# Performance work log

Hardware: AMD Instinct MI355X
Metric: run time of the kernel (lower is better)

## Reference

```python
import jax, jax.numpy as jnp
import numpy as np

EPS_BN = 1e-5
EPS_NORM = 1e-12


def _l2norm_c(x):
    # F.normalize over channel dim (dim=1) of [n, d, h, w]
    n = jnp.sqrt(jnp.sum(x * x, axis=1, keepdims=True))
    return x / jnp.maximum(n, EPS_NORM)


def setup_inputs() -> dict:
    key = jax.random.key(0)
    ks = jax.random.split(key, 8)
    g, p, d, h, w = 64, 64, 512, 24, 8
    hw = h * w
    return {
        "gal_fea": jax.random.normal(ks[0], (g, d, h, w), dtype=jnp.float32),
        "prob_fea": jax.random.normal(ks[1], (p, d, h, w), dtype=jnp.float32),
        "bn_weight": jax.random.uniform(ks[2], (1,), dtype=jnp.float32) + 0.5,
        "bn_bias": jax.random.uniform(ks[3], (1,), dtype=jnp.float32) - 0.5,
        "bn_mean": jnp.zeros((1,), dtype=jnp.float32),
        "bn_var": jnp.ones((1,), dtype=jnp.float32),
        "fc_weight": jax.random.normal(ks[4], (1, 2 * hw), dtype=jnp.float32) * 0.05,
        "fc_bias": jax.random.normal(ks[5], (1,), dtype=jnp.float32) * 0.05,
        "lbn_weight": jax.random.uniform(ks[6], (1,), dtype=jnp.float32) + 0.5,
        "lbn_bias": jax.random.uniform(ks[7], (1,), dtype=jnp.float32) - 0.5,
        "lbn_mean": jnp.zeros((1,), dtype=jnp.float32),
        "lbn_var": jnp.ones((1,), dtype=jnp.float32),
    }


def reference(gal_fea, prob_fea, bn_weight, bn_bias, bn_mean, bn_var,
              fc_weight, fc_bias, lbn_weight, lbn_bias, lbn_mean, lbn_var):
    g, d, h, w = gal_fea.shape
    p = prob_fea.shape[0]
    hw = h * w

    # L2-normalize over channels, flatten spatial dims
    gal = _l2norm_c(gal_fea).reshape(g, d, hw)              # [g, d, j]
    ker = _l2norm_c(prob_fea).transpose(0, 2, 3, 1).reshape(p, hw, d)  # [p, i, d]

    # cosine-similarity cross-correlation: s[g,p,i,j] = <probe pos i, gallery pos j>
    s = jnp.einsum('pid,gdj->gpij', ker, gal)               # [g, p, hw, hw]

    # dual spatial max-pool: max over probe positions, max over gallery positions
    score = jnp.concatenate([s.max(axis=2), s.max(axis=3)], axis=-1)  # [g, p, 2*hw]

    # eval-mode BatchNorm1d(1): scalar affine broadcast over all elements
    score = (score - bn_mean) / jnp.sqrt(bn_var + EPS_BN) * bn_weight + bn_bias

    # fc: Linear(2*hw, 1)
    score = jnp.einsum('gpk,ok->gpo', score, fc_weight)[..., 0] + fc_bias[0]  # [g, p]

    # eval-mode logit BatchNorm1d(1): scalar affine
    score = (score - lbn_mean) / jnp.sqrt(lbn_var + EPS_BN) * lbn_weight + lbn_bias

    return jax.nn.sigmoid(score / 10.0)
```

## Files before the change

kernel.cpp:

```cpp
#include <hip/hip_runtime.h>

#define HW 192
#define DD 512
#define GG 64
#define PP 64
#define SLAB 98304

typedef __attribute__((ext_vector_type(4))) float floatx4;
typedef __attribute__((ext_vector_type(2))) long long2_t;

typedef __attribute__((address_space(3))) unsigned int lds_u32;
typedef const __attribute__((address_space(1))) unsigned int glb_u32;

__device__ __forceinline__ void gload_lds16(const void* g, void* l) {
  __builtin_amdgcn_global_load_lds((glb_u32*)g, (lds_u32*)l, 16, 0, 0);
}

__global__ __launch_bounds__(512, 2) void norm_kernel(
    const float* __restrict__ gal, const float* __restrict__ prob,
    unsigned char* __restrict__ ws) {
  int b = blockIdx.x;
  int s = b / 12;
  int q = b - s * 12;
  const float* in = (s < GG) ? (gal + (size_t)s * DD * HW)
                             : (prob + (size_t)(s - GG) * DD * HW);
  unsigned char* out = ws + (size_t)s * SLAB;
  int pos0 = q * 16;
  int t = threadIdx.x;

  __shared__ float T[16][524];
  __shared__ float sqa[128][17];
  __shared__ float sq2[16][17];
  __shared__ float scl[16];

  {
    int cq = t >> 2;
    int quad = t & 3;
    float p0 = 0.f, p1 = 0.f, p2 = 0.f, p3 = 0.f;
#pragma unroll
    for (int cb = 0; cb < 4; ++cb) {
      int c = cb * 128 + cq;
      const float4 v = *(const float4*)(in + (size_t)c * HW + pos0 + quad * 4);
      T[quad * 4 + 0][c] = v.x;
      T[quad * 4 + 1][c] = v.y;
      T[quad * 4 + 2][c] = v.z;
      T[quad * 4 + 3][c] = v.w;
      p0 += v.x * v.x; p1 += v.y * v.y; p2 += v.z * v.z; p3 += v.w * v.w;
    }
    sqa[cq][quad * 4 + 0] = p0;
    sqa[cq][quad * 4 + 1] = p1;
    sqa[cq][quad * 4 + 2] = p2;
    sqa[cq][quad * 4 + 3] = p3;
  }
  __syncthreads();
  if (t < 256) {
    int g2 = t >> 4, pos = t & 15;
    float v = 0.f;
#pragma unroll
    for (int r = 0; r < 8; ++r) v += sqa[g2 * 8 + r][pos];
    sq2[g2][pos] = v;
  }
  __syncthreads();
  if (t < 16) {
    float v = 0.f;
#pragma unroll
    for (int r = 0; r < 16; ++r) v += sq2[r][t];
    scl[t] = 1.f / fmaxf(sqrtf(v), 1e-12f);
  }
  __syncthreads();

  {
    int kc = t & 3;
    int pos = (t >> 2) & 15;
    int kb2 = t >> 6;
    float sc = scl[pos];
    int base = kb2 * 64 + kc * 8;
    const float4 r0 = *(const float4*)&T[pos][base + 0];
    const float4 r1 = *(const float4*)&T[pos][base + 4];
    const float4 r2 = *(const float4*)&T[pos][base + 32];
    const float4 r3 = *(const float4*)&T[pos][base + 36];
    uint4 u;
    u.x = __builtin_amdgcn_cvt_pk_fp8_f32(r0.x * sc, r0.y * sc, 0, false);
    u.x = __builtin_amdgcn_cvt_pk_fp8_f32(r0.z * sc, r0.w * sc, u.x, true);
    u.y = __builtin_amdgcn_cvt_pk_fp8_f32(r1.x * sc, r1.y * sc, 0, false);
    u.y = __builtin_amdgcn_cvt_pk_fp8_f32(r1.z * sc, r1.w * sc, u.y, true);
    u.z = __builtin_amdgcn_cvt_pk_fp8_f32(r2.x * sc, r2.y * sc, 0, false);
    u.z = __builtin_amdgcn_cvt_pk_fp8_f32(r2.z * sc, r2.w * sc, u.z, true);
    u.w = __builtin_amdgcn_cvt_pk_fp8_f32(r3.x * sc, r3.y * sc, 0, false);
    u.w = __builtin_amdgcn_cvt_pk_fp8_f32(r3.z * sc, r3.w * sc, u.w, true);
    *(uint4*)(out + (size_t)kb2 * 12288 + (size_t)(pos0 + pos) * 64 + kc * 16) = u;
  }
}

__global__ __launch_bounds__(256, 2) void qaconv_gemm(
    const unsigned char* __restrict__ ws, const float* __restrict__ fcw,
    const float* __restrict__ bnw, const float* __restrict__ bnb,
    const float* __restrict__ bnm, const float* __restrict__ bnv,
    const float* __restrict__ fcb, const float* __restrict__ lw,
    const float* __restrict__ lb, const float* __restrict__ lm,
    const float* __restrict__ lv, float* __restrict__ out) {
  int bid = blockIdx.x;
  int sb = bid >> 6, li = bid & 63;
  int g = ((sb >> 3) << 3) + (li >> 3);
  int p = ((sb & 7) << 3) + (li & 7);
  const unsigned char* Bsrc = ws + (size_t)g * SLAB;
  const unsigned char* Asrc = ws + (size_t)(GG + p) * SLAB;

  __shared__ unsigned char A_lds[2][12288];
  __shared__ unsigned char B_lds[2][12288];
  __shared__ float colpart[2][HW];
  __shared__ float rowpart[2][HW];
  __shared__ float redbuf[4][2];

  int tid = threadIdx.x;
  int lane = tid & 63;
  int wave = tid >> 6;
  int wi = wave >> 1, wj = wave & 1;
  int l15 = lane & 15, l4 = lane >> 4;

  floatx4 acc[6][6];
#pragma unroll
  for (int a = 0; a < 6; ++a)
#pragma unroll
    for (int c = 0; c < 6; ++c) acc[a][c] = (floatx4){0.f, 0.f, 0.f, 0.f};

  int mIdx[3];
  int mOff[3];
#pragma unroll
  for (int s = 0; s < 3; ++s) {
    int m = tid + s * 256;
    mIdx[s] = m;
    mOff[s] = (m >> 2) * 64 + ((((m & 3) ^ ((m >> 3) & 3))) << 4);
  }

#define STAGE(KB2, BUF)                                             \
  do {                                                              \
    _Pragma("unroll") for (int s_ = 0; s_ < 3; ++s_) {              \
      size_t go = (size_t)(KB2)*12288 + (size_t)mOff[s_];           \
      gload_lds16(Asrc + go, &A_lds[BUF][mIdx[s_] * 16]);           \
      gload_lds16(Bsrc + go, &B_lds[BUF][mIdx[s_] * 16]);           \
    }                                                               \
  } while (0)

  STAGE(0, 0);
  __syncthreads();

  int sw = (l4 ^ ((l15 >> 1) & 3)) << 4;
  int aB = (wi * 96 + l15) * 64 + sw;
  int bB = (wj * 96 + l15) * 64 + sw;

  for (int kb2 = 0; kb2 < 8; ++kb2) {
    int cur = kb2 & 1;
    if (kb2 < 7) STAGE(kb2 + 1, cur ^ 1);

    long2_t a2[6];
#pragma unroll
    for (int it = 0; it < 6; ++it)
      a2[it] = *(const long2_t*)&A_lds[cur][aB + it * 1024];
#pragma unroll
    for (int jt = 0; jt < 6; ++jt) {
      long2_t b2 = *(const long2_t*)&B_lds[cur][bB + jt * 1024];
#pragma unroll
      for (int it = 0; it < 6; ++it)
        acc[it][jt] = __builtin_amdgcn_mfma_f32_16x16x32_fp8_fp8(a2[it].x, b2.x, acc[it][jt], 0, 0, 0);
#pragma unroll
      for (int it = 0; it < 6; ++it)
        acc[it][jt] = __builtin_amdgcn_mfma_f32_16x16x32_fp8_fp8(a2[it].y, b2.y, acc[it][jt], 0, 0, 0);
    }
    __syncthreads();
  }
#undef STAGE

  float cm[6];
  float rm[6][4];
#pragma unroll
  for (int jt = 0; jt < 6; ++jt) cm[jt] = -3.4e38f;
#pragma unroll
  for (int it = 0; it < 6; ++it)
#pragma unroll
    for (int r = 0; r < 4; ++r) rm[it][r] = -3.4e38f;
#pragma unroll
  for (int it = 0; it < 6; ++it)
#pragma unroll
    for (int jt = 0; jt < 6; ++jt)
#pragma unroll
      for (int r = 0; r < 4; ++r) {
        float v = acc[it][jt][r];
        cm[jt] = fmaxf(cm[jt], v);
        rm[it][r] = fmaxf(rm[it][r], v);
      }

#pragma unroll
  for (int jt = 0; jt < 6; ++jt) {
    float v = cm[jt];
    v = fmaxf(v, __shfl_xor(v, 16, 64));
    v = fmaxf(v, __shfl_xor(v, 32, 64));
    if (lane < 16) colpart[wi][wj * 96 + jt * 16 + lane] = v;
  }
#pragma unroll
  for (int it = 0; it < 6; ++it)
#pragma unroll
    for (int r = 0; r < 4; ++r) {
      float v = rm[it][r];
      v = fmaxf(v, __shfl_xor(v, 1, 64));
      v = fmaxf(v, __shfl_xor(v, 2, 64));
      v = fmaxf(v, __shfl_xor(v, 4, 64));
      v = fmaxf(v, __shfl_xor(v, 8, 64));
      if (l15 == 0) rowpart[wj][wi * 96 + it * 16 + l4 * 4 + r] = v;
    }
  __syncthreads();

  float part = 0.f, wpart = 0.f;
  if (tid < HW) {
    float cmax = fmaxf(colpart[0][tid], colpart[1][tid]);
    float rmax = fmaxf(rowpart[0][tid], rowpart[1][tid]);
    float w1 = fcw[tid], w2 = fcw[HW + tid];
    part = cmax * w1 + rmax * w2;
    wpart = w1 + w2;
  }
#pragma unroll
  for (int off = 32; off > 0; off >>= 1) {
    part += __shfl_down(part, off, 64);
    wpart += __shfl_down(wpart, off, 64);
  }
  if (lane == 0) { redbuf[wave][0] = part; redbuf[wave][1] = wpart; }
  __syncthreads();
  if (tid == 0) {
    float s = redbuf[0][0] + redbuf[1][0] + redbuf[2][0] + redbuf[3][0];
    float wsum = redbuf[0][1] + redbuf[1][1] + redbuf[2][1] + redbuf[3][1];
    float bnA = bnw[0] * rsqrtf(bnv[0] + 1e-5f);
    float bnB = bnb[0] - bnm[0] * bnA;
    float sc = bnA * s + bnB * wsum + fcb[0];
    float lA = lw[0] * rsqrtf(lv[0] + 1e-5f);
    sc = (sc - lm[0]) * lA + lb[0];
    out[g * PP + p] = 1.f / (1.f + __expf(-sc * 0.1f));
  }
}

extern "C" void kernel_launch(void* const* d_in, const int* in_sizes, int n_in,
                              void* d_out, int out_size, void* d_ws, size_t ws_size,
                              hipStream_t stream) {
  const float* gal  = (const float*)d_in[0];
  const float* prob = (const float*)d_in[1];
  const float* bnw  = (const float*)d_in[2];
  const float* bnb  = (const float*)d_in[3];
  const float* bnm  = (const float*)d_in[4];
  const float* bnv  = (const float*)d_in[5];
  const float* fcw  = (const float*)d_in[6];
  const float* fcb  = (const float*)d_in[7];
  const float* lw   = (const float*)d_in[8];
  const float* lb   = (const float*)d_in[9];
  const float* lm   = (const float*)d_in[10];
  const float* lv   = (const float*)d_in[11];
  unsigned char* ws = (unsigned char*)d_ws;
  float* out = (float*)d_out;

  hipLaunchKernelGGL(norm_kernel, dim3(1536), dim3(512), 0, stream, gal, prob, ws);
  hipLaunchKernelGGL(qaconv_gemm, dim3(GG * PP), dim3(256), 0, stream, ws, fcw,
                     bnw, bnb, bnm, bnv, fcb, lw, lb, lm, lv, out);
}
```

Before: 229.9 us.

## Switch fp8 GEMM to 32x32x64 scaled MFMA with matching fp8 layout

Replaces the 16x16x32 fp8 MFMA tiling (6x6 tiles per wave) with the gfx950 32x32x64 scaled f8f6f4 MFMA (3x3 tiles per wave), using unit scales. The norm kernel's fp8 packing order and the LDS read offsets change so each lane loads 32 contiguous k-bytes. The row/column max epilogue is rewritten for the 32x32 accumulator layout. The aim is fewer MFMA issues and LDS reads per k-step, at the cost of a more intricate layout mapping that must stay consistent between the two kernels.

```diff
diff --git a/kernel.cpp b/kernel.cpp
--- a/kernel.cpp
+++ b/kernel.cpp
@@ -6,8 +6,9 @@
 #define PP 64
 #define SLAB 98304
 
-typedef __attribute__((ext_vector_type(4))) float floatx4;
-typedef __attribute__((ext_vector_type(2))) long long2_t;
+typedef __attribute__((ext_vector_type(4))) int intx4;
+typedef __attribute__((ext_vector_type(8))) int intx8;
+typedef __attribute__((ext_vector_type(16))) float floatx16;
 
 typedef __attribute__((address_space(3))) unsigned int lds_u32;
 typedef const __attribute__((address_space(1))) unsigned int glb_u32;
@@ -74,11 +75,11 @@
     int pos = (t >> 2) & 15;
     int kb2 = t >> 6;
     float sc = scl[pos];
-    int base = kb2 * 64 + kc * 8;
+    int base = kb2 * 64 + kc * 16;
     const float4 r0 = *(const float4*)&T[pos][base + 0];
     const float4 r1 = *(const float4*)&T[pos][base + 4];
-    const float4 r2 = *(const float4*)&T[pos][base + 32];
-    const float4 r3 = *(const float4*)&T[pos][base + 36];
+    const float4 r2 = *(const float4*)&T[pos][base + 8];
+    const float4 r3 = *(const float4*)&T[pos][base + 12];
     uint4 u;
     u.x = __builtin_amdgcn_cvt_pk_fp8_f32(r0.x * sc, r0.y * sc, 0, false);
     u.x = __builtin_amdgcn_cvt_pk_fp8_f32(r0.z * sc, r0.w * sc, u.x, true);
@@ -116,13 +117,13 @@
   int lane = tid & 63;
   int wave = tid >> 6;
   int wi = wave >> 1, wj = wave & 1;
-  int l15 = lane & 15, l4 = lane >> 4;
-
-  floatx4 acc[6][6];
-#pragma unroll
-  for (int a = 0; a < 6; ++a)
-#pragma unroll
-    for (int c = 0; c < 6; ++c) acc[a][c] = (floatx4){0.f, 0.f, 0.f, 0.f};
+  int l31 = lane & 31;
+
+  floatx16 acc[3][3];
+#pragma unroll
+  for (int a = 0; a < 3; ++a)
+#pragma unroll
+    for (int c = 0; c < 3; ++c) acc[a][c] = (floatx16)(0.f);
 
   int mIdx[3];
   int mOff[3];
@@ -145,68 +146,69 @@
   STAGE(0, 0);
   __syncthreads();
 
-  int sw = (l4 ^ ((l15 >> 1) & 3)) << 4;
-  int aB = (wi * 96 + l15) * 64 + sw;
-  int bB = (wj * 96 + l15) * 64 + sw;
+  int xk = (lane >> 1) & 3;
+  int h2 = (lane >> 5) << 1;
+  int slotB0 = (h2 ^ xk) << 4;
+  int aO[3], bO[3];
+#pragma unroll
+  for (int ta = 0; ta < 3; ++ta) aO[ta] = (wi * 96 + ta * 32 + l31) * 64 + slotB0;
+#pragma unroll
+  for (int tc = 0; tc < 3; ++tc) bO[tc] = (wj * 96 + tc * 32 + l31) * 64 + slotB0;
+
+  const int sc8 = 0x7f7f7f7f;
 
   for (int kb2 = 0; kb2 < 8; ++kb2) {
     int cur = kb2 & 1;
     if (kb2 < 7) STAGE(kb2 + 1, cur ^ 1);
 
-    long2_t a2[6];
-#pragma unroll
-    for (int it = 0; it < 6; ++it)
-      a2[it] = *(const long2_t*)&A_lds[cur][aB + it * 1024];
-#pragma unroll
-    for (int jt = 0; jt < 6; ++jt) {
-      long2_t b2 = *(const long2_t*)&B_lds[cur][bB + jt * 1024];
-#pragma unroll
-      for (int it = 0; it < 6; ++it)
-        acc[it][jt] = __builtin_amdgcn_mfma_f32_16x16x32_fp8_fp8(a2[it].x, b2.x, acc[it][jt], 0, 0, 0);
-#pragma unroll
-      for (int it = 0; it < 6; ++it)
-        acc[it][jt] = __builtin_amdgcn_mfma_f32_16x16x32_fp8_fp8(a2[it].y, b2.y, acc[it][jt], 0, 0, 0);
+    intx8 af[3];
+#pragma unroll
+    for (int ta = 0; ta < 3; ++ta) {
+      intx4 lo = *(const intx4*)&A_lds[cur][aO[ta]];
+      intx4 hi = *(const intx4*)&A_lds[cur][aO[ta] ^ 16];
+      intx8 v;
+      v[0] = lo.x; v[1] = lo.y; v[2] = lo.z; v[3] = lo.w;
+      v[4] = hi.x; v[5] = hi.y; v[6] = hi.z; v[7] = hi.w;
+      af[ta] = v;
+    }
+#pragma unroll
+    for (int tc = 0; tc < 3; ++tc) {
+      intx4 lo = *(const intx4*)&B_lds[cur][bO[tc]];
+      intx4 hi = *(const intx4*)&B_lds[cur][bO[tc] ^ 16];
+      intx8 bf;
+      bf[0] = lo.x; bf[1] = lo.y; bf[2] = lo.z; bf[3] = lo.w;
+      bf[4] = hi.x; bf[5] = hi.y; bf[6] = hi.z; bf[7] = hi.w;
+#pragma unroll
+      for (int ta = 0; ta < 3; ++ta)
+        acc[ta][tc] = __builtin_amdgcn_mfma_scale_f32_32x32x64_f8f6f4(
+            af[ta], bf, acc[ta][tc], 0, 0, 0, sc8, 0, sc8);
     }
     __syncthreads();
   }
 #undef STAGE
 
-  float cm[6];
-  float rm[6][4];
-#pragma unroll
-  for (int jt = 0; jt < 6; ++jt) cm[jt] = -3.4e38f;
-#pragma unroll
-  for (int it = 0; it < 6; ++it)
-#pragma unroll
-    for (int r = 0; r < 4; ++r) rm[it][r] = -3.4e38f;
-#pragma unroll
-  for (int it = 0; it < 6; ++it)
-#pragma unroll
-    for (int jt = 0; jt < 6; ++jt)
-#pragma unroll
-      for (int r = 0; r < 4; ++r) {
-        float v = acc[it][jt][r];
-        cm[jt] = fmaxf(cm[jt], v);
-        rm[it][r] = fmaxf(rm[it][r], v);
-      }
-
-#pragma unroll
-  for (int jt = 0; jt < 6; ++jt) {
-    float v = cm[jt];
-    v = fmaxf(v, __shfl_xor(v, 16, 64));
+#pragma unroll
+  for (int tc = 0; tc < 3; ++tc) {
+    float v = -3.4e38f;
+#pragma unroll
+    for (int ta = 0; ta < 3; ++ta)
+#pragma unroll
+      for (int r = 0; r < 16; ++r) v = fmaxf(v, acc[ta][tc][r]);
     v = fmaxf(v, __shfl_xor(v, 32, 64));
-    if (lane < 16) colpart[wi][wj * 96 + jt * 16 + lane] = v;
-  }
-#pragma unroll
-  for (int it = 0; it < 6; ++it)
-#pragma unroll
-    for (int r = 0; r < 4; ++r) {
-      float v = rm[it][r];
+    if (lane < 32) colpart[wi][wj * 96 + tc * 32 + lane] = v;
+  }
+#pragma unroll
+  for (int ta = 0; ta < 3; ++ta)
+#pragma unroll
+    for (int r = 0; r < 16; ++r) {
+      float v = fmaxf(fmaxf(acc[ta][0][r], acc[ta][1][r]), acc[ta][2][r]);
       v = fmaxf(v, __shfl_xor(v, 1, 64));
       v = fmaxf(v, __shfl_xor(v, 2, 64));
       v = fmaxf(v, __shfl_xor(v, 4, 64));
       v = fmaxf(v, __shfl_xor(v, 8, 64));
-      if (l15 == 0) rowpart[wj][wi * 96 + it * 16 + l4 * 4 + r] = v;
+      v = fmaxf(v, __shfl_xor(v, 16, 64));
+      if (l31 == 0)
+        rowpart[wj][wi * 96 + ta * 32 + (r & 3) + 8 * (r >> 2) + ((lane >> 5) << 2)] = v;
     }
   __syncthreads();
 
```

Result: slower. 247.1 us (+7.5%).

## Store fp8 operands in MFMA fragment order and load directly into registers

Applied to the files above, without the earlier changes.

The norm kernel now writes fp8 data in the exact per-lane fragment layout the MFMA expects, 16 contiguous bytes per lane per 16-row tile. The GEMM kernel drops the LDS staging buffers, swizzle and barriers, and loads fragments straight from global memory into registers with a two-deep register double buffer. This removes LDS traffic and block-wide synchronisation. In exchange each wave fetches its own A/B fragments from L2, which duplicates global reads across waves, and register pressure rises.

```diff
diff --git a/kernel.cpp b/kernel.cpp
--- a/kernel.cpp
+++ b/kernel.cpp
@@ -8,13 +8,6 @@
 
 typedef __attribute__((ext_vector_type(4))) float floatx4;
 typedef __attribute__((ext_vector_type(2))) long long2_t;
-
-typedef __attribute__((address_space(3))) unsigned int lds_u32;
-typedef const __attribute__((address_space(1))) unsigned int glb_u32;
-
-__device__ __forceinline__ void gload_lds16(const void* g, void* l) {
-  __builtin_amdgcn_global_load_lds((glb_u32*)g, (lds_u32*)l, 16, 0, 0);
-}
 
 __global__ __launch_bounds__(512, 2) void norm_kernel(
     const float* __restrict__ gal, const float* __restrict__ prob,
@@ -70,11 +63,12 @@
   __syncthreads();
 
   {
-    int kc = t & 3;
-    int pos = (t >> 2) & 15;
     int kb2 = t >> 6;
+    int lane = t & 63;
+    int l4 = lane >> 4;
+    int pos = lane & 15;
     float sc = scl[pos];
-    int base = kb2 * 64 + kc * 8;
+    int base = kb2 * 64 + l4 * 8;
     const float4 r0 = *(const float4*)&T[pos][base + 0];
     const float4 r1 = *(const float4*)&T[pos][base + 4];
     const float4 r2 = *(const float4*)&T[pos][base + 32];
@@ -88,7 +82,7 @@
     u.z = __builtin_amdgcn_cvt_pk_fp8_f32(r2.z * sc, r2.w * sc, u.z, true);
     u.w = __builtin_amdgcn_cvt_pk_fp8_f32(r3.x * sc, r3.y * sc, 0, false);
     u.w = __builtin_amdgcn_cvt_pk_fp8_f32(r3.z * sc, r3.w * sc, u.w, true);
-    *(uint4*)(out + (size_t)kb2 * 12288 + (size_t)(pos0 + pos) * 64 + kc * 16) = u;
+    *(uint4*)(out + (size_t)kb2 * 12288 + (size_t)q * 1024 + (size_t)lane * 16) = u;
   }
 }
 
@@ -106,8 +100,6 @@
   const unsigned char* Bsrc = ws + (size_t)g * SLAB;
   const unsigned char* Asrc = ws + (size_t)(GG + p) * SLAB;
 
-  __shared__ unsigned char A_lds[2][12288];
-  __shared__ unsigned char B_lds[2][12288];
   __shared__ float colpart[2][HW];
   __shared__ float rowpart[2][HW];
   __shared__ float redbuf[4][2];
@@ -124,52 +116,41 @@
 #pragma unroll
     for (int c = 0; c < 6; ++c) acc[a][c] = (floatx4){0.f, 0.f, 0.f, 0.f};
 
-  int mIdx[3];
-  int mOff[3];
-#pragma unroll
-  for (int s = 0; s < 3; ++s) {
-    int m = tid + s * 256;
-    mIdx[s] = m;
-    mOff[s] = (m >> 2) * 64 + ((((m & 3) ^ ((m >> 3) & 3))) << 4);
-  }
-
-#define STAGE(KB2, BUF)                                             \
-  do {                                                              \
-    _Pragma("unroll") for (int s_ = 0; s_ < 3; ++s_) {              \
-      size_t go = (size_t)(KB2)*12288 + (size_t)mOff[s_];           \
-      gload_lds16(Asrc + go, &A_lds[BUF][mIdx[s_] * 16]);           \
-      gload_lds16(Bsrc + go, &B_lds[BUF][mIdx[s_] * 16]);           \
-    }                                                               \
+  const unsigned char* aP = Asrc + (size_t)(wi * 6) * 1024 + (size_t)lane * 16;
+  const unsigned char* bP = Bsrc + (size_t)(wj * 6) * 1024 + (size_t)lane * 16;
+
+#define LOADF(AD, BD, KB)                                                 \
+  do {                                                                    \
+    _Pragma("unroll") for (int it_ = 0; it_ < 6; ++it_) {                 \
+      AD[it_] = *(const long2_t*)(aP + (size_t)(KB)*12288 + it_ * 1024);  \
+      BD[it_] = *(const long2_t*)(bP + (size_t)(KB)*12288 + it_ * 1024);  \
+    }                                                                     \
   } while (0)
 
-  STAGE(0, 0);
-  __syncthreads();
-
-  int sw = (l4 ^ ((l15 >> 1) & 3)) << 4;
-  int aB = (wi * 96 + l15) * 64 + sw;
-  int bB = (wj * 96 + l15) * 64 + sw;
-
-  for (int kb2 = 0; kb2 < 8; ++kb2) {
-    int cur = kb2 & 1;
-    if (kb2 < 7) STAGE(kb2 + 1, cur ^ 1);
-
-    long2_t a2[6];
-#pragma unroll
-    for (int it = 0; it < 6; ++it)
-      a2[it] = *(const long2_t*)&A_lds[cur][aB + it * 1024];
-#pragma unroll
-    for (int jt = 0; jt < 6; ++jt) {
-      long2_t b2 = *(const long2_t*)&B_lds[cur][bB + jt * 1024];
-#pragma unroll
-      for (int it = 0; it < 6; ++it)
-        acc[it][jt] = __builtin_amdgcn_mfma_f32_16x16x32_fp8_fp8(a2[it].x, b2.x, acc[it][jt], 0, 0, 0);
-#pragma unroll
-      for (int it = 0; it < 6; ++it)
-        acc[it][jt] = __builtin_amdgcn_mfma_f32_16x16x32_fp8_fp8(a2[it].y, b2.y, acc[it][jt], 0, 0, 0);
-    }
-    __syncthreads();
-  }
-#undef STAGE
+#define MFMAB(AD, BD)                                                      \
+  do {                                                                     \
+    _Pragma("unroll") for (int jt_ = 0; jt_ < 6; ++jt_) {                  \
+      long2_t bb = BD[jt_];                                                \
+      _Pragma("unroll") for (int it_ = 0; it_ < 6; ++it_)                  \
+          acc[it_][jt_] = __builtin_amdgcn_mfma_f32_16x16x32_fp8_fp8(      \
+              AD[it_].x, bb.x, acc[it_][jt_], 0, 0, 0);                    \
+      _Pragma("unroll") for (int it_ = 0; it_ < 6; ++it_)                  \
+          acc[it_][jt_] = __builtin_amdgcn_mfma_f32_16x16x32_fp8_fp8(      \
+              AD[it_].y, bb.y, acc[it_][jt_], 0, 0, 0);                    \
+    }                                                                      \
+  } while (0)
+
+  long2_t aC[6], bC[6], aN[6], bN[6];
+  LOADF(aC, bC, 0);
+#pragma unroll 1
+  for (int kb2 = 0; kb2 < 8; kb2 += 2) {
+    LOADF(aN, bN, kb2 + 1);
+    MFMAB(aC, bC);
+    if (kb2 < 6) LOADF(aC, bC, kb2 + 2);
+    MFMAB(aN, bN);
+  }
+#undef LOADF
+#undef MFMAB
 
   float cm[6];
   float rm[6][4];
```

Measured after the change: 216.4 us. 1.06x faster.
